# Kernel tuning notes

Hardware: AMD Instinct MI355X
Metric: run time of the kernel (lower is better)

Reference implementation:

```python
import jax, jax.numpy as jnp
import numpy as np

OW = 80                # cfg.out_size[1]
POS_THRESHOLD = 0.005  # cfg.pos_threshold
LN_EPS = 1e-5


def setup_inputs() -> dict:
    key = jax.random.key(0)
    ks = jax.random.split(key, 6)
    B, C, T, N = 16, 1024, 64, 12
    NFG = NFR = NFG_ONE = 1024
    s = 0.02
    return {
        "x": jax.random.normal(ks[0], (B, C, T, N), dtype=jnp.float32),
        "A": jax.random.uniform(ks[1], (B, T, N, 4), dtype=jnp.float32),
        "w_theta": jax.random.normal(ks[2], (NFG, NFR), dtype=jnp.float32) * s,
        "b_theta": jnp.zeros((NFR,), dtype=jnp.float32),
        "w_phi": jax.random.normal(ks[3], (NFG, NFR), dtype=jnp.float32) * s,
        "b_phi": jnp.zeros((NFR,), dtype=jnp.float32),
        "w_gcn": jax.random.normal(ks[4], (NFG, NFG_ONE), dtype=jnp.float32) * s,
        "ln_w": jnp.ones((N, NFG_ONE), dtype=jnp.float32),
        "ln_b": jnp.zeros((N, NFG_ONE), dtype=jnp.float32),
    }


def reference(x, A, w_theta, b_theta, w_phi, b_phi, w_gcn, ln_w, ln_b):
    B, C, T, N = x.shape
    # box centers -> pairwise euclidean distances per (B*T) frame
    boxes = A.reshape(-1, 4)
    cx = (boxes[:, 0] + boxes[:, 2]) * 0.5
    cy = (boxes[:, 1] + boxes[:, 3]) * 0.5
    pos = jnp.stack([cx, cy], axis=-1).reshape(B * T, N, 2)
    sq = jnp.sum(pos * pos, axis=2)  # [BT, N]
    d2 = sq[:, :, None] - 2.0 * jnp.einsum('bnc,bmc->bnm', pos, pos) + sq[:, None, :]
    dist = jnp.sqrt(jnp.maximum(d2, 0.0))  # clamp tiny negatives from fp error
    position_mask = dist > POS_THRESHOLD * OW  # [BT, N, N]

    # features: [B, C, T, N] -> [BT, N, C]
    feat = jnp.transpose(x, (0, 2, 3, 1)).reshape(B * T, N, C)
    theta = feat @ w_theta + b_theta  # [BT, N, NFR]
    phi = feat @ w_phi + b_phi        # [BT, N, NFR]
    scale = 1.0 / jnp.sqrt(jnp.asarray(theta.shape[-1], dtype=feat.dtype))
    logits = jnp.einsum('bnf,bmf->bnm', theta, phi) * scale
    logits = jnp.where(position_mask, -jnp.inf, logits)
    relation_graph = jax.nn.softmax(logits, axis=2)  # [BT, N, N]

    # graph conv: aggregate then project (no bias)
    agg = jnp.einsum('bnm,bmc->bnc', relation_graph, feat) @ w_gcn  # [BT, N, NFG_ONE]

    # LayerNorm over the last two dims [N, NFG_ONE]
    mu = jnp.mean(agg, axis=(1, 2), keepdims=True)
    var = jnp.var(agg, axis=(1, 2), keepdims=True)
    normed = (agg - mu) / jnp.sqrt(var + LN_EPS) * ln_w + ln_b
    out = jax.nn.relu(normed)
    return out, relation_graph
```

## Files before the change

### kernel.cpp

```cpp
#include <hip/hip_runtime.h>
#include <math.h>
#include <stdint.h>

#define NDIM   12
#define KDIM   1024
#define BT_TOT 1024
#define M_TOT  (BT_TOT * NDIM)
#define OUT_MAIN (M_TOT * KDIM)
#define MASK_TH 0.4f
#define LN_EPS 1e-5f

typedef float f32x4 __attribute__((ext_vector_type(4)));
typedef short bf16x8 __attribute__((ext_vector_type(8)));
typedef short bf16x4 __attribute__((ext_vector_type(4)));

__device__ __forceinline__ float bf2f(unsigned short u) {
    return __uint_as_float(((unsigned int)u) << 16);
}
__device__ __forceinline__ unsigned short f2bf(float f) {
    unsigned int u = __float_as_uint(f);
    return (unsigned short)((u + 0x7FFFu + ((u >> 16) & 1u)) >> 16);
}
__device__ __forceinline__ void gld16(const void* g, void* l) {
    __builtin_amdgcn_global_load_lds(
        (const __attribute__((address_space(1))) unsigned int*)g,
        (__attribute__((address_space(3))) unsigned int*)l, 16, 0, 0);
}

__global__ __launch_bounds__(256)
void prep_kernel(const float* __restrict__ x,   const float* __restrict__ wth,
                 const float* __restrict__ wph, const float* __restrict__ bth,
                 const float* __restrict__ wg,
                 unsigned short* __restrict__ wth_b, unsigned short* __restrict__ wph_b,
                 unsigned short* __restrict__ wgT,   float* __restrict__ vbuf,
                 unsigned short* __restrict__ featB)
{
    const int bid = blockIdx.x, tid = threadIdx.x;
    __shared__ float tileF[64][33];

    if (bid < 1024) {
        const float* src = bid < 512 ? wth : wph;
        unsigned short* dst = bid < 512 ? wth_b : wph_b;
        const size_t off = (size_t)(bid & 511) * 2048 + (size_t)tid * 8;
        const float4 a = *(const float4*)(src + off);
        const float4 b = *(const float4*)(src + off + 4);
        unsigned short o[8] = {f2bf(a.x), f2bf(a.y), f2bf(a.z), f2bf(a.w),
                               f2bf(b.x), f2bf(b.y), f2bf(b.z), f2bf(b.w)};
        *(uint4*)(dst + off) = *(const uint4*)o;
    } else if (bid < 2048) {
        const int b2 = bid - 1024;
        const int o0 = (b2 & 31) * 32, c0 = (b2 >> 5) * 32;
        const int tx = tid & 31, ty = tid >> 5;
        #pragma unroll
        for (int i = 0; i < 4; ++i) {
            const int r = ty + i * 8;
            tileF[r][tx] = wg[(size_t)(c0 + r) * KDIM + o0 + tx];
        }
        __syncthreads();
        #pragma unroll
        for (int i = 0; i < 4; ++i) {
            const int r = ty + i * 8;
            wgT[(size_t)(o0 + r) * KDIM + c0 + tx] = f2bf(tileF[tx][r]);
        }
    } else if (bid < 2304) {
        const int b3 = bid - 2048;
        const int lane = tid & 63, w = tid >> 6;
        const int j = b3 * 4 + w;
        const float4* row = (const float4*)(wph + (size_t)j * KDIM);
        const float4* bt4 = (const float4*)bth;
        float s = 0.f;
        #pragma unroll
        for (int i = 0; i < 4; ++i) {
            const float4 a = row[lane + i * 64], b = bt4[lane + i * 64];
            s += a.x * b.x + a.y * b.y + a.z * b.z + a.w * b.w;
        }
        #pragma unroll
        for (int msk = 32; msk >= 1; msk >>= 1) s += __shfl_xor(s, msk, 64);
        if (lane == 0) vbuf[j] = s;
    } else {
        const int b4 = bid - 2304;
        const int px = b4 % 24;
        const int rest = b4 / 24;
        const int cx = rest & 15, b = rest >> 4;
        const int p0 = px * 32, c0 = cx * 64;
        const float* src = x + (size_t)b * KDIM * 768;
        #pragma unroll
        for (int i = 0; i < 8; ++i) {
            const int cl = (tid >> 5) + i * 8;
            tileF[cl][tid & 31] = src[(size_t)(c0 + cl) * 768 + p0 + (tid & 31)];
        }
        __syncthreads();
        unsigned short* dst = featB + ((size_t)b * 768 + p0) * KDIM;
        #pragma unroll
        for (int i = 0; i < 8; ++i) {
            const int pp = (tid >> 6) + i * 4;
            const int cl = tid & 63;
            dst[(size_t)pp * KDIM + c0 + cl] = f2bf(tileF[cl][pp]);
        }
    }
}

template<bool SWZ>
__global__ __launch_bounds__(256)
void gemm_kernel(const unsigned short* __restrict__ A,
                 const unsigned short* __restrict__ B0, const unsigned short* __restrict__ B1,
                 unsigned short* __restrict__ C0, unsigned short* __restrict__ C1)
{
    int m0, n0, zz;
    if (SWZ) {
        const int bid = blockIdx.x;
        const int c = bid & 7, s = bid >> 3;
        const int n = s & 7, mm = (s >> 3) % 12, z = s / 96;
        m0 = (c * 12 + mm) * 128; n0 = n * 128; zz = z;
    } else {
        m0 = blockIdx.y * 128; n0 = blockIdx.x * 128; zz = blockIdx.z;
    }
    const unsigned short* B = zz ? B1 : B0;
    unsigned short* C       = zz ? C1 : C0;

    const int tid = threadIdx.x, lane = tid & 63, wid = tid >> 6;
    const int wr = wid >> 1, wc = wid & 1;

    __shared__ __align__(16) unsigned short As[128 * 64];
    __shared__ __align__(16) unsigned short Bs[128 * 64];

    f32x4 acc[4][4] = {};

    const int srow_w = wid * 8 + (lane >> 3);
    const int schunk = lane & 7;

    for (int k0 = 0; k0 < KDIM; k0 += 64) {
        #pragma unroll
        for (int i = 0; i < 4; ++i) {
            const int row = srow_w + i * 32;
            const int gchunk = schunk ^ (row & 7);
            const char* srcA = (const char*)A + ((size_t)(m0 + row) * KDIM + k0) * 2 + gchunk * 16;
            const char* srcB = (const char*)B + ((size_t)(n0 + row) * KDIM + k0) * 2 + gchunk * 16;
            char* la = (char*)As + i * 4096 + wid * 1024;
            char* lb = (char*)Bs + i * 4096 + wid * 1024;
            gld16(srcA, la);
            gld16(srcB, lb);
        }
        __syncthreads();

        #pragma unroll
        for (int ks = 0; ks < 2; ++ks) {
            bf16x8 af[4], bfr[4];
            const int cch = ks * 4 + (lane >> 4);
            #pragma unroll
            for (int mi = 0; mi < 4; ++mi) {
                const int r = wr * 64 + (lane & 15) + mi * 16;
                af[mi] = *(const bf16x8*)((const char*)As + r * 128 + ((cch ^ (r & 7)) * 16));
            }
            #pragma unroll
            for (int ni = 0; ni < 4; ++ni) {
                const int r = wc * 64 + (lane & 15) + ni * 16;
                bfr[ni] = *(const bf16x8*)((const char*)Bs + r * 128 + ((cch ^ (r & 7)) * 16));
            }
            #pragma unroll
            for (int mi = 0; mi < 4; ++mi)
                #pragma unroll
                for (int ni = 0; ni < 4; ++ni)
                    acc[mi][ni] = __builtin_amdgcn_mfma_f32_16x16x32_bf16(
                        af[mi], bfr[ni], acc[mi][ni], 0, 0, 0);
        }
        __syncthreads();
    }

    #pragma unroll
    for (int mi = 0; mi < 4; ++mi) {
        const int gr0 = m0 + wr * 64 + mi * 16 + (lane >> 4) * 4;
        #pragma unroll
        for (int ni = 0; ni < 4; ++ni) {
            const int gc = n0 + wc * 64 + ni * 16 + (lane & 15);
            const f32x4 v = acc[mi][ni];
            #pragma unroll
            for (int reg = 0; reg < 4; ++reg)
                C[(size_t)(gr0 + reg) * KDIM + gc] = f2bf(v[reg]);
        }
    }
}

__global__ __launch_bounds__(256)
void relf_kernel(const unsigned short* __restrict__ G,
                 const unsigned short* __restrict__ featB,
                 const unsigned short* __restrict__ H,
                 const float* __restrict__ Abox, const float* __restrict__ vbuf,
                 const float* __restrict__ lnw, const float* __restrict__ lnb,
                 float* __restrict__ out)
{
    const int f = blockIdx.x, tid = threadIdx.x, lane = tid & 63, w = tid >> 6;
    __shared__ float Lred[4][16][16];
    __shared__ float relS[12][12];
    __shared__ float cxS[12], cyS[12], sqS[12];
    __shared__ float qred[4][12];
    __shared__ float rs[2][256];

    if (tid < 12) {
        const float4 box = *(const float4*)(Abox + ((size_t)f * 12 + tid) * 4);
        const float cx = (box.x + box.z) * 0.5f, cy = (box.y + box.w) * 0.5f;
        cxS[tid] = cx; cyS[tid] = cy; sqS[tid] = cx * cx + cy * cy;
    }

    const int r = lane & 15, rr = r < 12 ? r : 0;
    const int kq = (lane >> 4) * 8;
    const unsigned short* gG = G + (size_t)(f * 12 + rr) * KDIM;
    const unsigned short* gF = featB + (size_t)(f * 12 + rr) * KDIM;
    f32x4 acc = {};
    #pragma unroll
    for (int s8 = 0; s8 < 8; ++s8) {
        const int k0 = (w * 8 + s8) * 32 + kq;
        const bf16x8 a = *(const bf16x8*)(gG + k0);
        const bf16x8 b = *(const bf16x8*)(gF + k0);
        acc = __builtin_amdgcn_mfma_f32_16x16x32_bf16(a, b, acc, 0, 0, 0);
    }
    {
        const int row0 = (lane >> 4) * 4, col = lane & 15;
        #pragma unroll
        for (int reg = 0; reg < 4; ++reg) Lred[w][row0 + reg][col] = acc[reg];
    }

    const int c0 = tid * 4;
    {
        const float4 v4 = *(const float4*)(vbuf + c0);
        float qp[12];
        #pragma unroll
        for (int m = 0; m < 12; ++m) {
            const bf16x4 fm = *(const bf16x4*)(featB + (size_t)(f * 12 + m) * KDIM + c0);
            qp[m] = bf2f((unsigned short)fm[0]) * v4.x + bf2f((unsigned short)fm[1]) * v4.y
                  + bf2f((unsigned short)fm[2]) * v4.z + bf2f((unsigned short)fm[3]) * v4.w;
        }
        #pragma unroll
        for (int msk = 32; msk >= 1; msk >>= 1)
            #pragma unroll
            for (int m = 0; m < 12; ++m) qp[m] += __shfl_xor(qp[m], msk, 64);
        if (lane == 0) {
            #pragma unroll
            for (int m = 0; m < 12; ++m) qred[w][m] = qp[m];
        }
    }
    __syncthreads();

    if (tid < 12) {
        const int n = tid;
        float l[12], mx = -3.4e38f;
        #pragma unroll
        for (int m = 0; m < 12; ++m) {
            const float L = Lred[0][n][m] + Lred[1][n][m] + Lred[2][n][m] + Lred[3][n][m];
            const float qm = qred[0][m] + qred[1][m] + qred[2][m] + qred[3][m];
            float val = (L + qm) * 0.03125f;
            const float d2 = sqS[n] - 2.f * (cxS[n] * cxS[m] + cyS[n] * cyS[m]) + sqS[m];
            const float dist = sqrtf(fmaxf(d2, 0.f));
            if (dist > MASK_TH) val = -INFINITY;
            l[m] = val; mx = fmaxf(mx, val);
        }
        float s = 0.f, e[12];
        #pragma unroll
        for (int m = 0; m < 12; ++m) { e[m] = expf(l[m] - mx); s += e[m]; }
        const float inv = 1.f / s;
        float* orel = out + (size_t)OUT_MAIN + (size_t)f * 144 + n * 12;
        #pragma unroll
        for (int m = 0; m < 12; ++m) {
            const float rv = e[m] * inv;
            relS[n][m] = rv;
            orel[m] = rv;
        }
    }
    __syncthreads();

    float h[12][4];
    #pragma unroll
    for (int m = 0; m < 12; ++m) {
        const bf16x4 h4 = *(const bf16x4*)(H + (size_t)(f * 12 + m) * KDIM + c0);
        #pragma unroll
        for (int j = 0; j < 4; ++j) h[m][j] = bf2f((unsigned short)h4[j]);
    }
    float a2[12][4];
    float s = 0.f, s2 = 0.f;
    #pragma unroll
    for (int n = 0; n < 12; ++n) {
        float rn[12];
        #pragma unroll
        for (int m = 0; m < 12; ++m) rn[m] = relS[n][m];
        #pragma unroll
        for (int j = 0; j < 4; ++j) {
            float a = 0.f;
            #pragma unroll
            for (int m = 0; m < 12; ++m) a = fmaf(rn[m], h[m][j], a);
            a2[n][j] = a; s += a; s2 += a * a;
        }
    }
    rs[0][tid] = s; rs[1][tid] = s2;
    __syncthreads();
    for (int o = 128; o > 0; o >>= 1) {
        if (tid < o) { rs[0][tid] += rs[0][tid + o]; rs[1][tid] += rs[1][tid + o]; }
        __syncthreads();
    }
    const float mu = rs[0][0] * (1.f / 12288.f);
    const float var = rs[1][0] * (1.f / 12288.f) - mu * mu;
    const float rstd = rsqrtf(var + LN_EPS);

    #pragma unroll
    for (int n = 0; n < 12; ++n) {
        const float4 wv = *(const float4*)(lnw + (size_t)n * KDIM + c0);
        const float4 bv = *(const float4*)(lnb + (size_t)n * KDIM + c0);
        float4 ov;
        ov.x = fmaxf(fmaf((a2[n][0] - mu) * rstd, wv.x, bv.x), 0.f);
        ov.y = fmaxf(fmaf((a2[n][1] - mu) * rstd, wv.y, bv.y), 0.f);
        ov.z = fmaxf(fmaf((a2[n][2] - mu) * rstd, wv.z, bv.z), 0.f);
        ov.w = fmaxf(fmaf((a2[n][3] - mu) * rstd, wv.w, bv.w), 0.f);
        *(float4*)(out + (size_t)(f * 12 + n) * KDIM + c0) = ov;
    }
}

extern "C" void kernel_launch(void* const* d_in, const int* in_sizes, int n_in,
                              void* d_out, int out_size, void* d_ws, size_t ws_size,
                              hipStream_t stream) {
    const float* x   = (const float*)d_in[0];
    const float* A   = (const float*)d_in[1];
    const float* wth = (const float*)d_in[2];
    const float* bth = (const float*)d_in[3];
    const float* wph = (const float*)d_in[4];
    const float* wg  = (const float*)d_in[6];
    const float* lnw = (const float*)d_in[7];
    const float* lnb = (const float*)d_in[8];
    float* out = (float*)d_out;

    char* ws = (char*)d_ws;
    const size_t MB = 1ull << 20;
    unsigned short* featB = (unsigned short*)(ws);
    unsigned short* G     = (unsigned short*)(ws + 24 * MB);
    unsigned short* H     = (unsigned short*)(ws + 48 * MB);
    unsigned short* wth_b = (unsigned short*)(ws + 72 * MB);
    unsigned short* wph_b = (unsigned short*)(ws + 74 * MB);
    unsigned short* wgT   = (unsigned short*)(ws + 76 * MB);
    unsigned short* MtB   = (unsigned short*)(ws + 78 * MB);
    float* vbuf = (float*)(ws + 80 * MB);

    prep_kernel<<<8448, 256, 0, stream>>>(x, wth, wph, bth, wg,
                                          wth_b, wph_b, wgT, vbuf, featB);
    gemm_kernel<false><<<dim3(8, 8, 1), 256, 0, stream>>>(
        wph_b, wth_b, wth_b, MtB, MtB);
    gemm_kernel<true><<<1536, 256, 0, stream>>>(
        featB, MtB, wgT, G, H);
    relf_kernel<<<BT_TOT, 256, 0, stream>>>(G, featB, H, A, vbuf, lnw, lnb, out);
}
```

Baseline: 220.6 us.

## Fold weight-product GEMM into prep kernel and fuse q-vector into relation MFMA loop

The separate bf16 conversion of w_theta/w_phi and the small 1024x1024 Wphi·Wthetaᵀ GEMM launch are removed. The first 64 prep blocks now compute that product directly from fp32 weights, converting to bf16 on the fly, which drops one kernel launch and the intermediate bf16 weight buffers. The relation kernel computes the per-node bias term from the feature fragments it already loads for the MFMA, replacing a second featB read and a 12-way shuffle reduction. Its block-to-frame mapping is also interleaved to spread memory accesses. A risk is that the 64 GEMM blocks, which use a single-buffered LDS loop with no prefetch, become a long tail inside prep.

```diff
diff --git a/kernel.cpp b/kernel.cpp
--- a/kernel.cpp
+++ b/kernel.cpp
@@ -31,24 +31,95 @@
 void prep_kernel(const float* __restrict__ x,   const float* __restrict__ wth,
                  const float* __restrict__ wph, const float* __restrict__ bth,
                  const float* __restrict__ wg,
-                 unsigned short* __restrict__ wth_b, unsigned short* __restrict__ wph_b,
-                 unsigned short* __restrict__ wgT,   float* __restrict__ vbuf,
-                 unsigned short* __restrict__ featB)
+                 unsigned short* __restrict__ wgT, float* __restrict__ vbuf,
+                 unsigned short* __restrict__ featB, unsigned short* __restrict__ MtB)
 {
     const int bid = blockIdx.x, tid = threadIdx.x;
-    __shared__ float tileF[64][33];
-
-    if (bid < 1024) {
-        const float* src = bid < 512 ? wth : wph;
-        unsigned short* dst = bid < 512 ? wth_b : wph_b;
-        const size_t off = (size_t)(bid & 511) * 2048 + (size_t)tid * 8;
-        const float4 a = *(const float4*)(src + off);
-        const float4 b = *(const float4*)(src + off + 4);
-        unsigned short o[8] = {f2bf(a.x), f2bf(a.y), f2bf(a.z), f2bf(a.w),
-                               f2bf(b.x), f2bf(b.y), f2bf(b.z), f2bf(b.w)};
-        *(uint4*)(dst + off) = *(const uint4*)o;
-    } else if (bid < 2048) {
-        const int b2 = bid - 1024;
+    __shared__ __align__(16) char ldsb[16384];
+
+    if (bid < 64) {
+        const int m0 = (bid >> 3) * 128, n0 = (bid & 7) * 128;
+        const int lane = tid & 63, wid = tid >> 6;
+        const int wr = wid >> 1, wc = wid & 1;
+        unsigned short* As = (unsigned short*)ldsb;
+        unsigned short* Bs = As + 4096;
+        f32x4 acc[4][4] = {};
+        const int row = tid >> 1, half = tid & 1;
+
+        for (int k0 = 0; k0 < KDIM; k0 += 32) {
+            const float* ga = wph + (size_t)(m0 + row) * KDIM + k0 + half * 16;
+            const float* gb = wth + (size_t)(n0 + row) * KDIM + k0 + half * 16;
+            unsigned short pa[16], pb[16];
+            #pragma unroll
+            for (int j = 0; j < 4; ++j) {
+                const float4 va = ((const float4*)ga)[j];
+                const float4 vb = ((const float4*)gb)[j];
+                pa[j*4+0] = f2bf(va.x); pa[j*4+1] = f2bf(va.y);
+                pa[j*4+2] = f2bf(va.z); pa[j*4+3] = f2bf(va.w);
+                pb[j*4+0] = f2bf(vb.x); pb[j*4+1] = f2bf(vb.y);
+                pb[j*4+2] = f2bf(vb.z); pb[j*4+3] = f2bf(vb.w);
+            }
+            const int le = row * 32 + half * 16;
+            *(uint4*)&As[le]     = ((const uint4*)pa)[0];
+            *(uint4*)&As[le + 8] = ((const uint4*)pa)[1];
+            *(uint4*)&Bs[le]     = ((const uint4*)pb)[0];
+            *(uint4*)&Bs[le + 8] = ((const uint4*)pb)[1];
+            __syncthreads();
+
+            bf16x8 af[4], bfr[4];
+            const int rA = wr * 64 + (lane & 15);
+            const int rB = wc * 64 + (lane & 15);
+            const int kq = (lane >> 4) * 8;
+            #pragma unroll
+            for (int mi = 0; mi < 4; ++mi)
+                af[mi] = *(const bf16x8*)&As[(rA + mi * 16) * 32 + kq];
+            #pragma unroll
+            for (int ni = 0; ni < 4; ++ni)
+                bfr[ni] = *(const bf16x8*)&Bs[(rB + ni * 16) * 32 + kq];
+            #pragma unroll
+            for (int mi = 0; mi < 4; ++mi)
+                #pragma unroll
+                for (int ni = 0; ni < 4; ++ni)
+                    acc[mi][ni] = __builtin_amdgcn_mfma_f32_16x16x32_bf16(
+                        af[mi], bfr[ni], acc[mi][ni], 0, 0, 0);
+            __syncthreads();
+        }
+        #pragma unroll
+        for (int mi = 0; mi < 4; ++mi) {
+            const int gr0 = m0 + wr * 64 + mi * 16 + ((tid & 63) >> 4) * 4;
+            #pragma unroll
+            for (int ni = 0; ni < 4; ++ni) {
+                const int gc = n0 + wc * 64 + ni * 16 + (tid & 15);
+                const f32x4 v = acc[mi][ni];
+                #pragma unroll
+                for (int reg = 0; reg < 4; ++reg)
+                    MtB[(size_t)(gr0 + reg) * KDIM + gc] = f2bf(v[reg]);
+            }
+        }
+    } else if (bid < 6208) {
+        float (*tileF)[33] = (float(*)[33])ldsb;
+        const int b4 = bid - 64;
+        const int px = b4 % 24;
+        const int rest = b4 / 24;
+        const int cx = rest & 15, b = rest >> 4;
+        const int p0 = px * 32, c0 = cx * 64;
+        const float* src = x + (size_t)b * KDIM * 768;
+        #pragma unroll
+        for (int i = 0; i < 8; ++i) {
+            const int cl = (tid >> 5) + i * 8;
+            tileF[cl][tid & 31] = src[(size_t)(c0 + cl) * 768 + p0 + (tid & 31)];
+        }
+        __syncthreads();
+        unsigned short* dst = featB + ((size_t)b * 768 + p0) * KDIM;
+        #pragma unroll
+        for (int i = 0; i < 8; ++i) {
+            const int pp = (tid >> 6) + i * 4;
+            const int cl = tid & 63;
+            dst[(size_t)pp * KDIM + c0 + cl] = f2bf(tileF[cl][pp]);
+        }
+    } else if (bid < 7232) {
+        float (*tileF)[33] = (float(*)[33])ldsb;
+        const int b2 = bid - 6208;
         const int o0 = (b2 & 31) * 32, c0 = (b2 >> 5) * 32;
         const int tx = tid & 31, ty = tid >> 5;
         #pragma unroll
@@ -62,8 +133,8 @@
             const int r = ty + i * 8;
             wgT[(size_t)(o0 + r) * KDIM + c0 + tx] = f2bf(tileF[tx][r]);
         }
-    } else if (bid < 2304) {
-        const int b3 = bid - 2048;
+    } else {
+        const int b3 = bid - 7232;
         const int lane = tid & 63, w = tid >> 6;
         const int j = b3 * 4 + w;
         const float4* row = (const float4*)(wph + (size_t)j * KDIM);
@@ -77,46 +148,20 @@
         #pragma unroll
         for (int msk = 32; msk >= 1; msk >>= 1) s += __shfl_xor(s, msk, 64);
         if (lane == 0) vbuf[j] = s;
-    } else {
-        const int b4 = bid - 2304;
-        const int px = b4 % 24;
-        const int rest = b4 / 24;
-        const int cx = rest & 15, b = rest >> 4;
-        const int p0 = px * 32, c0 = cx * 64;
-        const float* src = x + (size_t)b * KDIM * 768;
-        #pragma unroll
-        for (int i = 0; i < 8; ++i) {
-            const int cl = (tid >> 5) + i * 8;
-            tileF[cl][tid & 31] = src[(size_t)(c0 + cl) * 768 + p0 + (tid & 31)];
-        }
-        __syncthreads();
-        unsigned short* dst = featB + ((size_t)b * 768 + p0) * KDIM;
-        #pragma unroll
-        for (int i = 0; i < 8; ++i) {
-            const int pp = (tid >> 6) + i * 4;
-            const int cl = tid & 63;
-            dst[(size_t)pp * KDIM + c0 + cl] = f2bf(tileF[cl][pp]);
-        }
-    }
-}
-
-template<bool SWZ>
+    }
+}
+
 __global__ __launch_bounds__(256)
 void gemm_kernel(const unsigned short* __restrict__ A,
                  const unsigned short* __restrict__ B0, const unsigned short* __restrict__ B1,
                  unsigned short* __restrict__ C0, unsigned short* __restrict__ C1)
 {
-    int m0, n0, zz;
-    if (SWZ) {
-        const int bid = blockIdx.x;
-        const int c = bid & 7, s = bid >> 3;
-        const int n = s & 7, mm = (s >> 3) % 12, z = s / 96;
-        m0 = (c * 12 + mm) * 128; n0 = n * 128; zz = z;
-    } else {
-        m0 = blockIdx.y * 128; n0 = blockIdx.x * 128; zz = blockIdx.z;
-    }
-    const unsigned short* B = zz ? B1 : B0;
-    unsigned short* C       = zz ? C1 : C0;
+    const int bid = blockIdx.x;
+    const int c = bid & 7, s = bid >> 3;
+    const int n = s & 7, mm = (s >> 3) % 12, z = s / 96;
+    const int m0 = (c * 12 + mm) * 128, n0 = n * 128;
+    const unsigned short* B = z ? B1 : B0;
+    unsigned short* C       = z ? C1 : C0;
 
     const int tid = threadIdx.x, lane = tid & 63, wid = tid >> 6;
     const int wr = wid >> 1, wc = wid & 1;
@@ -189,7 +234,9 @@
                  const float* __restrict__ lnw, const float* __restrict__ lnb,
                  float* __restrict__ out)
 {
-    const int f = blockIdx.x, tid = threadIdx.x, lane = tid & 63, w = tid >> 6;
+    const int bid = blockIdx.x;
+    const int f = ((bid & 7) << 7) + (bid >> 3);
+    const int tid = threadIdx.x, lane = tid & 63, w = tid >> 6;
     __shared__ float Lred[4][16][16];
     __shared__ float relS[12][12];
     __shared__ float cxS[12], cyS[12], sqS[12];
@@ -207,37 +254,27 @@
     const unsigned short* gG = G + (size_t)(f * 12 + rr) * KDIM;
     const unsigned short* gF = featB + (size_t)(f * 12 + rr) * KDIM;
     f32x4 acc = {};
+    float qp = 0.f;
     #pragma unroll
     for (int s8 = 0; s8 < 8; ++s8) {
         const int k0 = (w * 8 + s8) * 32 + kq;
         const bf16x8 a = *(const bf16x8*)(gG + k0);
         const bf16x8 b = *(const bf16x8*)(gF + k0);
         acc = __builtin_amdgcn_mfma_f32_16x16x32_bf16(a, b, acc, 0, 0, 0);
-    }
+        const float4 v0 = *(const float4*)(vbuf + k0);
+        const float4 v1 = *(const float4*)(vbuf + k0 + 4);
+        qp += bf2f((unsigned short)b[0]) * v0.x + bf2f((unsigned short)b[1]) * v0.y
+            + bf2f((unsigned short)b[2]) * v0.z + bf2f((unsigned short)b[3]) * v0.w
+            + bf2f((unsigned short)b[4]) * v1.x + bf2f((unsigned short)b[5]) * v1.y
+            + bf2f((unsigned short)b[6]) * v1.z + bf2f((unsigned short)b[7]) * v1.w;
+    }
+    qp += __shfl_xor(qp, 16, 64);
+    qp += __shfl_xor(qp, 32, 64);
+    if (lane < 12) qred[w][lane] = qp;
     {
         const int row0 = (lane >> 4) * 4, col = lane & 15;
         #pragma unroll
         for (int reg = 0; reg < 4; ++reg) Lred[w][row0 + reg][col] = acc[reg];
-    }
-
-    const int c0 = tid * 4;
-    {
-        const float4 v4 = *(const float4*)(vbuf + c0);
-        float qp[12];
-        #pragma unroll
-        for (int m = 0; m < 12; ++m) {
-            const bf16x4 fm = *(const bf16x4*)(featB + (size_t)(f * 12 + m) * KDIM + c0);
-            qp[m] = bf2f((unsigned short)fm[0]) * v4.x + bf2f((unsigned short)fm[1]) * v4.y
-                  + bf2f((unsigned short)fm[2]) * v4.z + bf2f((unsigned short)fm[3]) * v4.w;
-        }
-        #pragma unroll
-        for (int msk = 32; msk >= 1; msk >>= 1)
-            #pragma unroll
-            for (int m = 0; m < 12; ++m) qp[m] += __shfl_xor(qp[m], msk, 64);
-        if (lane == 0) {
-            #pragma unroll
-            for (int m = 0; m < 12; ++m) qred[w][m] = qp[m];
-        }
     }
     __syncthreads();
 
@@ -268,6 +305,7 @@
     }
     __syncthreads();
 
+    const int c0 = tid * 4;
     float h[12][4];
     #pragma unroll
     for (int m = 0; m < 12; ++m) {
@@ -331,17 +369,12 @@
     unsigned short* featB = (unsigned short*)(ws);
     unsigned short* G     = (unsigned short*)(ws + 24 * MB);
     unsigned short* H     = (unsigned short*)(ws + 48 * MB);
-    unsigned short* wth_b = (unsigned short*)(ws + 72 * MB);
-    unsigned short* wph_b = (unsigned short*)(ws + 74 * MB);
-    unsigned short* wgT   = (unsigned short*)(ws + 76 * MB);
-    unsigned short* MtB   = (unsigned short*)(ws + 78 * MB);
-    float* vbuf = (float*)(ws + 80 * MB);
-
-    prep_kernel<<<8448, 256, 0, stream>>>(x, wth, wph, bth, wg,
-                                          wth_b, wph_b, wgT, vbuf, featB);
-    gemm_kernel<false><<<dim3(8, 8, 1), 256, 0, stream>>>(
-        wph_b, wth_b, wth_b, MtB, MtB);
-    gemm_kernel<true><<<1536, 256, 0, stream>>>(
-        featB, MtB, wgT, G, H);
+    unsigned short* wgT   = (unsigned short*)(ws + 72 * MB);
+    unsigned short* MtB   = (unsigned short*)(ws + 74 * MB);
+    float* vbuf = (float*)(ws + 76 * MB);
+
+    prep_kernel<<<7488, 256, 0, stream>>>(x, wth, wph, bth, wg,
+                                          wgT, vbuf, featB, MtB);
+    gemm_kernel<<<1536, 256, 0, stream>>>(featB, MtB, wgT, G, H);
     relf_kernel<<<BT_TOT, 256, 0, stream>>>(G, featB, H, A, vbuf, lnw, lnb, out);
 }
```

Result: slower. 226.3 us (+2.6%).
